# Optimization experiments

Hardware: AMD Instinct MI355X
Metric: run time of the kernel (lower is better)

Reference implementation:

```python
import jax, jax.numpy as jnp
import numpy as np

B, N, U = 16, 1024, 64  # batch, nodes, num_units
ALPHA = 0.2  # LeakyReLU negative slope
NEG = -9e15


def setup_inputs() -> dict:
    key = jax.random.key(0)
    ks = jax.random.split(key, 7)
    X = jax.random.normal(ks[0], (B, N, U), dtype=jnp.float32)
    state = jax.random.normal(ks[1], (B, N, U), dtype=jnp.float32)
    # random sparse adjacency (avg degree ~32) with self-loops
    adj = (jax.random.uniform(ks[2], (N, N)) < 32.0 / N).astype(jnp.float32)
    adj = jnp.maximum(adj, jnp.eye(N, dtype=jnp.float32))
    def xavier(k, shape):
        fan_in, fan_out = shape
        s = 1.414 * np.sqrt(6.0 / (fan_in + fan_out))
        return jax.random.uniform(k, shape, jnp.float32, -s, s)
    W1 = xavier(ks[3], (2 * U, 2 * U))   # gat_1: in 2U -> out 2U
    a1 = xavier(ks[4], (4 * U, 1))       # attention vector, 2*out
    W2 = xavier(ks[5], (2 * U, U))       # gat_2: in 2U -> out U
    a2 = xavier(ks[6], (2 * U, 1))
    return {"X": X, "state": state, "adj": adj, "W1": W1, "a1": a1, "W2": W2, "a2": a2}


def _gat_layer(x, adj, W, a):
    # x: [b,n,f_in], W: [f_in,F], a: [2F,1]
    h = jnp.einsum('bnf,fo->bno', x, W)              # [b,n,F]
    F_out = W.shape[1]
    s_src = h @ a[:F_out, 0]                         # [b,n] contribution of node i
    s_dst = h @ a[F_out:, 0]                         # [b,n] contribution of node j
    e = jax.nn.leaky_relu(s_src[:, :, None] + s_dst[:, None, :], ALPHA)  # [b,n,n]
    e = jnp.where(adj[None, :, :] > 0, e, NEG)
    att = jax.nn.softmax(e, axis=2)                  # masked softmax over neighbors j
    return jnp.einsum('bij,bjf->bif', att, h)        # [b,n,F]


def reference(X, state, adj, W1, a1, W2, a2):
    X1 = jnp.concatenate([X, state], axis=2)         # [b,n,2U]
    gv = jax.nn.sigmoid(_gat_layer(X1, adj, W1, a1)) # [b,n,2U]
    r, z = jnp.split(gv, 2, axis=2)                  # each [b,n,U]
    X2 = jnp.concatenate([X, r * state], axis=2)
    h_t1 = jnp.tanh(_gat_layer(X2, adj, W2, a2))     # [b,n,U]
    new_h = z * state + (1.0 - z) * h_t1
    return new_h
```

## Files before the change

kernel.cpp:

```cpp
#include <hip/hip_runtime.h>

#define BB 16
#define NN 1024
#define LALPHA 0.2f
#define MAXD 192

__global__ void build_csr(const float* __restrict__ adj, int* __restrict__ deg,
                          int* __restrict__ cols) {
    __shared__ int cnt;
    int i = blockIdx.x;
    if (threadIdx.x == 0) cnt = 0;
    __syncthreads();
    for (int j = threadIdx.x; j < NN; j += blockDim.x) {
        if (adj[(size_t)i * NN + j] > 0.0f) {
            int p = atomicAdd(&cnt, 1);
            if (p < MAXD) cols[(size_t)i * MAXD + p] = j;
        }
    }
    __syncthreads();
    if (threadIdx.x == 0) deg[i] = cnt < MAXD ? cnt : MAXD;
}

template <int FOUT, int RB>
__global__ void gemm_score(const float* __restrict__ A0, const float* __restrict__ A1,
                           const float* __restrict__ W, const float* __restrict__ avec,
                           float* __restrict__ h, float* __restrict__ s_src,
                           float* __restrict__ s_dst) {
    constexpr int TFN = FOUT / 4;
    constexpr int NT = (RB / 4) * TFN;
    __shared__ float xs[RB][132];
    int t = threadIdx.x;
    int tf = t % TFN, tr = t / TFN;
    int f0 = tf * 4, r0 = tr * 4;
    int base = blockIdx.x * RB;

    for (int idx = t; idx < RB * 32; idx += NT) {
        int r = idx >> 5, c = (idx & 31) * 4;
        float4 v = (c < 64) ? *(const float4*)(A0 + (size_t)(base + r) * 64 + c)
                            : *(const float4*)(A1 + (size_t)(base + r) * 64 + (c - 64));
        xs[r][c] = v.x; xs[r][c + 1] = v.y; xs[r][c + 2] = v.z; xs[r][c + 3] = v.w;
    }
    __syncthreads();

    float acc[4][4] = {};
    for (int k = 0; k < 128; k += 4) {
        float4 xv[4], wv[4];
#pragma unroll
        for (int i = 0; i < 4; i++) xv[i] = *(const float4*)&xs[r0 + i][k];
#pragma unroll
        for (int i = 0; i < 4; i++) wv[i] = *(const float4*)(W + (size_t)(k + i) * FOUT + f0);
#pragma unroll
        for (int i = 0; i < 4; i++) {
            float xr[4] = {xv[i].x, xv[i].y, xv[i].z, xv[i].w};
#pragma unroll
            for (int kk = 0; kk < 4; kk++) {
                acc[i][0] += xr[kk] * wv[kk].x;
                acc[i][1] += xr[kk] * wv[kk].y;
                acc[i][2] += xr[kk] * wv[kk].z;
                acc[i][3] += xr[kk] * wv[kk].w;
            }
        }
    }

    float a_s[4], a_d[4];
#pragma unroll
    for (int i = 0; i < 4; i++) {
        a_s[i] = avec[f0 + i];
        a_d[i] = avec[FOUT + f0 + i];
    }
#pragma unroll
    for (int i = 0; i < 4; i++) {
        int m = base + r0 + i;
        *(float4*)(h + (size_t)m * FOUT + f0) =
            make_float4(acc[i][0], acc[i][1], acc[i][2], acc[i][3]);
        float ps = acc[i][0] * a_s[0] + acc[i][1] * a_s[1] + acc[i][2] * a_s[2] + acc[i][3] * a_s[3];
        float pd = acc[i][0] * a_d[0] + acc[i][1] * a_d[1] + acc[i][2] * a_d[2] + acc[i][3] * a_d[3];
#pragma unroll
        for (int o = TFN / 2; o >= 1; o >>= 1) {
            ps += __shfl_xor(ps, o);
            pd += __shfl_xor(pd, o);
        }
        if (tf == 0) {
            s_src[m] = ps;
            s_dst[m] = pd;
        }
    }
}

__global__ __launch_bounds__(256) void attn1_kernel(
    const int* __restrict__ deg, const int* __restrict__ cols,
    const float* __restrict__ h1, const float* __restrict__ s_src,
    const float* __restrict__ s_dst, const float* __restrict__ state,
    float* __restrict__ rstate, float* __restrict__ zbuf) {
    int wv = threadIdx.x >> 6;
    int lane = threadIdx.x & 63;
    int node = wv >> 1;
    int half = wv & 1;
    int bi = blockIdx.x * 2 + node;
    int i = bi & (NN - 1);
    int b = bi >> 10;
    int d = deg[i];
    float ssrc = s_src[bi];
    __shared__ float w[2][MAXD];
    __shared__ int cl[2][MAXD];

    float ev[3];
    float mx = -1e30f;
    int nslot = 0;
    for (int j = lane; j < d; j += 64, nslot++) {
        int c = cols[(size_t)i * MAXD + j];
        cl[node][j] = c;
        float e = ssrc + s_dst[b * NN + c];
        e = e > 0.f ? e : LALPHA * e;
        ev[nslot] = e;
        mx = fmaxf(mx, e);
    }
#pragma unroll
    for (int o = 32; o >= 1; o >>= 1) mx = fmaxf(mx, __shfl_xor(mx, o));
    float sum = 0.f;
    {
        int s = 0;
        for (int j = lane; j < d; j += 64, s++) {
            float p = __expf(ev[s] - mx);
            sum += p;
            w[node][j] = p;
        }
    }
#pragma unroll
    for (int o = 32; o >= 1; o >>= 1) sum += __shfl_xor(sum, o);
    float inv = 1.f / sum;

    const float* hb = h1 + (size_t)b * NN * 128 + half * 64;
    float acc = 0.f;
    int j = 0;
    for (; j + 1 < d; j += 2) {
        float w0 = w[node][j], w1 = w[node][j + 1];
        const float* p0 = hb + (size_t)cl[node][j] * 128;
        const float* p1 = hb + (size_t)cl[node][j + 1] * 128;
        acc += w0 * p0[lane] + w1 * p1[lane];
    }
    if (j < d) acc += w[node][j] * (hb + (size_t)cl[node][j] * 128)[lane];

    float g = 1.f / (1.f + __expf(-acc * inv));
    float st = state[(size_t)bi * 64 + lane];
    if (half == 0)
        rstate[(size_t)bi * 64 + lane] = g * st;
    else
        zbuf[(size_t)bi * 64 + lane] = g;
}

__global__ __launch_bounds__(256) void attn2_kernel(
    const int* __restrict__ deg, const int* __restrict__ cols,
    const float* __restrict__ h2, const float* __restrict__ s_src,
    const float* __restrict__ s_dst, const float* __restrict__ state,
    const float* __restrict__ zbuf, float* __restrict__ out) {
    int wv = threadIdx.x >> 6;
    int lane = threadIdx.x & 63;
    int node = wv >> 1;
    int half = wv & 1;
    int bi = blockIdx.x * 2 + node;
    int i = bi & (NN - 1);
    int b = bi >> 10;
    int d = deg[i];
    float ssrc = s_src[bi];
    __shared__ float w[2][MAXD];
    __shared__ int cl[2][MAXD];
    __shared__ float part[2][64];

    float ev[3];
    float mx = -1e30f;
    int nslot = 0;
    for (int j = lane; j < d; j += 64, nslot++) {
        int c = cols[(size_t)i * MAXD + j];
        cl[node][j] = c;
        float e = ssrc + s_dst[b * NN + c];
        e = e > 0.f ? e : LALPHA * e;
        ev[nslot] = e;
        mx = fmaxf(mx, e);
    }
#pragma unroll
    for (int o = 32; o >= 1; o >>= 1) mx = fmaxf(mx, __shfl_xor(mx, o));
    float sum = 0.f;
    {
        int s = 0;
        for (int j = lane; j < d; j += 64, s++) {
            float p = __expf(ev[s] - mx);
            sum += p;
            w[node][j] = p;
        }
    }
#pragma unroll
    for (int o = 32; o >= 1; o >>= 1) sum += __shfl_xor(sum, o);
    float inv = 1.f / sum;

    const float* hb = h2 + (size_t)b * NN * 64;
    float acc = 0.f;
    int j = half;
    for (; j + 2 < d; j += 4) {
        float w0 = w[node][j], w1 = w[node][j + 2];
        const float* p0 = hb + (size_t)cl[node][j] * 64;
        const float* p1 = hb + (size_t)cl[node][j + 2] * 64;
        acc += w0 * p0[lane] + w1 * p1[lane];
    }
    for (; j < d; j += 2) acc += w[node][j] * (hb + (size_t)cl[node][j] * 64)[lane];

    if (half == 1) part[node][lane] = acc;
    __syncthreads();
    if (half == 0) {
        acc += part[node][lane];
        float ht = tanhf(acc * inv);
        float z = zbuf[(size_t)bi * 64 + lane];
        float st = state[(size_t)bi * 64 + lane];
        out[(size_t)bi * 64 + lane] = z * st + (1.f - z) * ht;
    }
}

extern "C" void kernel_launch(void* const* d_in, const int* in_sizes, int n_in,
                              void* d_out, int out_size, void* d_ws, size_t ws_size,
                              hipStream_t stream) {
    const float* X     = (const float*)d_in[0];
    const float* state = (const float*)d_in[1];
    const float* adj   = (const float*)d_in[2];
    const float* W1    = (const float*)d_in[3];
    const float* a1    = (const float*)d_in[4];
    const float* W2    = (const float*)d_in[5];
    const float* a2    = (const float*)d_in[6];
    float* out = (float*)d_out;

    char* ws = (char*)d_ws;
    size_t off = 0;
    auto alloc = [&](size_t bytes) -> void* {
        void* p = ws + off;
        off = (off + bytes + 255) & ~(size_t)255;
        return p;
    };
    int*   deg    = (int*)alloc(NN * sizeof(int));
    int*   cols   = (int*)alloc((size_t)NN * MAXD * sizeof(int));
    float* h1     = (float*)alloc((size_t)BB * NN * 128 * sizeof(float));
    float* ssrc1  = (float*)alloc((size_t)BB * NN * sizeof(float));
    float* sdst1  = (float*)alloc((size_t)BB * NN * sizeof(float));
    float* rstate = (float*)alloc((size_t)BB * NN * 64 * sizeof(float));
    float* zbuf   = (float*)alloc((size_t)BB * NN * 64 * sizeof(float));
    float* h2     = (float*)alloc((size_t)BB * NN * 64 * sizeof(float));
    float* ssrc2  = (float*)alloc((size_t)BB * NN * sizeof(float));
    float* sdst2  = (float*)alloc((size_t)BB * NN * sizeof(float));

    const int M = BB * NN;

    build_csr<<<NN, 256, 0, stream>>>(adj, deg, cols);
    gemm_score<128, 32><<<M / 32, 256, 0, stream>>>(X, state, W1, a1, h1, ssrc1, sdst1);
    attn1_kernel<<<M / 2, 256, 0, stream>>>(deg, cols, h1, ssrc1, sdst1, state, rstate, zbuf);
    gemm_score<64, 64><<<M / 64, 256, 0, stream>>>(X, rstate, W2, a2, h2, ssrc2, sdst2);
    attn2_kernel<<<M / 2, 256, 0, stream>>>(deg, cols, h2, ssrc2, sdst2, state, zbuf, out);
}
```

Measured before the change: 160.2 us.

## Use one wave per node with float2 feature loads in attention kernels

Reassigns each node to a single 64-lane wave instead of two waves, with each lane accumulating two features via float2 loads. Pads neighbor lists to a multiple of four with zero weights to unroll the gather loop by four. This removes duplicated softmax computation across waves and widens memory accesses, at the cost of fewer concurrent waves per node and a block-level sync.

```diff
diff --git a/kernel.cpp b/kernel.cpp
--- a/kernel.cpp
+++ b/kernel.cpp
@@ -87,131 +87,138 @@
     }
 }
 
-__global__ __launch_bounds__(256) void attn1_kernel(
+__global__ __launch_bounds__(64) void attn1_kernel(
     const int* __restrict__ deg, const int* __restrict__ cols,
     const float* __restrict__ h1, const float* __restrict__ s_src,
     const float* __restrict__ s_dst, const float* __restrict__ state,
     float* __restrict__ rstate, float* __restrict__ zbuf) {
-    int wv = threadIdx.x >> 6;
-    int lane = threadIdx.x & 63;
-    int node = wv >> 1;
-    int half = wv & 1;
-    int bi = blockIdx.x * 2 + node;
+    int bi = blockIdx.x;
     int i = bi & (NN - 1);
     int b = bi >> 10;
+    int lane = threadIdx.x;
     int d = deg[i];
     float ssrc = s_src[bi];
-    __shared__ float w[2][MAXD];
-    __shared__ int cl[2][MAXD];
+    __shared__ float w[MAXD + 4];
+    __shared__ int cl[MAXD + 4];
 
     float ev[3];
     float mx = -1e30f;
-    int nslot = 0;
-    for (int j = lane; j < d; j += 64, nslot++) {
+    int s = 0;
+    for (int j = lane; j < d; j += 64, s++) {
         int c = cols[(size_t)i * MAXD + j];
-        cl[node][j] = c;
+        cl[j] = c;
         float e = ssrc + s_dst[b * NN + c];
         e = e > 0.f ? e : LALPHA * e;
-        ev[nslot] = e;
+        ev[s] = e;
         mx = fmaxf(mx, e);
     }
 #pragma unroll
     for (int o = 32; o >= 1; o >>= 1) mx = fmaxf(mx, __shfl_xor(mx, o));
     float sum = 0.f;
-    {
-        int s = 0;
-        for (int j = lane; j < d; j += 64, s++) {
-            float p = __expf(ev[s] - mx);
-            sum += p;
-            w[node][j] = p;
-        }
+    s = 0;
+    for (int j = lane; j < d; j += 64, s++) {
+        float p = __expf(ev[s] - mx);
+        w[j] = p;
+        sum += p;
     }
 #pragma unroll
     for (int o = 32; o >= 1; o >>= 1) sum += __shfl_xor(sum, o);
+    if (lane < 4) {
+        w[d + lane] = 0.f;
+        cl[d + lane] = 0;
+    }
+    __syncthreads();
     float inv = 1.f / sum;
 
-    const float* hb = h1 + (size_t)b * NN * 128 + half * 64;
-    float acc = 0.f;
-    int j = 0;
-    for (; j + 1 < d; j += 2) {
-        float w0 = w[node][j], w1 = w[node][j + 1];
-        const float* p0 = hb + (size_t)cl[node][j] * 128;
-        const float* p1 = hb + (size_t)cl[node][j + 1] * 128;
-        acc += w0 * p0[lane] + w1 * p1[lane];
-    }
-    if (j < d) acc += w[node][j] * (hb + (size_t)cl[node][j] * 128)[lane];
-
-    float g = 1.f / (1.f + __expf(-acc * inv));
-    float st = state[(size_t)bi * 64 + lane];
-    if (half == 0)
-        rstate[(size_t)bi * 64 + lane] = g * st;
-    else
-        zbuf[(size_t)bi * 64 + lane] = g;
-}
-
-__global__ __launch_bounds__(256) void attn2_kernel(
+    const float* hb = h1 + (size_t)b * NN * 128 + lane * 2;
+    int de4 = (d + 3) & ~3;
+    float ax = 0.f, ay = 0.f;
+    for (int j = 0; j < de4; j += 4) {
+        float2 r0 = *(const float2*)(hb + (size_t)cl[j] * 128);
+        float2 r1 = *(const float2*)(hb + (size_t)cl[j + 1] * 128);
+        float2 r2 = *(const float2*)(hb + (size_t)cl[j + 2] * 128);
+        float2 r3 = *(const float2*)(hb + (size_t)cl[j + 3] * 128);
+        float w0 = w[j], w1 = w[j + 1], w2 = w[j + 2], w3 = w[j + 3];
+        ax += w0 * r0.x + w1 * r1.x + w2 * r2.x + w3 * r3.x;
+        ay += w0 * r0.y + w1 * r1.y + w2 * r2.y + w3 * r3.y;
+    }
+    float gx = 1.f / (1.f + __expf(-ax * inv));
+    float gy = 1.f / (1.f + __expf(-ay * inv));
+    if (lane < 32) {
+        float2 st = *(const float2*)(state + (size_t)bi * 64 + lane * 2);
+        *(float2*)(rstate + (size_t)bi * 64 + lane * 2) = make_float2(gx * st.x, gy * st.y);
+    } else {
+        int l2 = lane - 32;
+        *(float2*)(zbuf + (size_t)bi * 64 + l2 * 2) = make_float2(gx, gy);
+    }
+}
+
+__global__ __launch_bounds__(64) void attn2_kernel(
     const int* __restrict__ deg, const int* __restrict__ cols,
     const float* __restrict__ h2, const float* __restrict__ s_src,
     const float* __restrict__ s_dst, const float* __restrict__ state,
     const float* __restrict__ zbuf, float* __restrict__ out) {
-    int wv = threadIdx.x >> 6;
-    int lane = threadIdx.x & 63;
-    int node = wv >> 1;
-    int half = wv & 1;
-    int bi = blockIdx.x * 2 + node;
+    int bi = blockIdx.x;
     int i = bi & (NN - 1);
     int b = bi >> 10;
+    int lane = threadIdx.x;
+    int half = lane >> 5;
+    int fl = lane & 31;
     int d = deg[i];
     float ssrc = s_src[bi];
-    __shared__ float w[2][MAXD];
-    __shared__ int cl[2][MAXD];
-    __shared__ float part[2][64];
+    __shared__ float w[MAXD + 4];
+    __shared__ int cl[MAXD + 4];
 
     float ev[3];
     float mx = -1e30f;
-    int nslot = 0;
-    for (int j = lane; j < d; j += 64, nslot++) {
+    int s = 0;
+    for (int j = lane; j < d; j += 64, s++) {
         int c = cols[(size_t)i * MAXD + j];
-        cl[node][j] = c;
+        cl[j] = c;
         float e = ssrc + s_dst[b * NN + c];
         e = e > 0.f ? e : LALPHA * e;
-        ev[nslot] = e;
+        ev[s] = e;
         mx = fmaxf(mx, e);
     }
 #pragma unroll
     for (int o = 32; o >= 1; o >>= 1) mx = fmaxf(mx, __shfl_xor(mx, o));
     float sum = 0.f;
-    {
-        int s = 0;
-        for (int j = lane; j < d; j += 64, s++) {
-            float p = __expf(ev[s] - mx);
-            sum += p;
-            w[node][j] = p;
-        }
+    s = 0;
+    for (int j = lane; j < d; j += 64, s++) {
+        float p = __expf(ev[s] - mx);
+        w[j] = p;
+        sum += p;
     }
 #pragma unroll
     for (int o = 32; o >= 1; o >>= 1) sum += __shfl_xor(sum, o);
+    if (lane < 4) {
+        w[d + lane] = 0.f;
+        cl[d + lane] = 0;
+    }
+    __syncthreads();
     float inv = 1.f / sum;
 
-    const float* hb = h2 + (size_t)b * NN * 64;
-    float acc = 0.f;
-    int j = half;
-    for (; j + 2 < d; j += 4) {
-        float w0 = w[node][j], w1 = w[node][j + 2];
-        const float* p0 = hb + (size_t)cl[node][j] * 64;
-        const float* p1 = hb + (size_t)cl[node][j + 2] * 64;
-        acc += w0 * p0[lane] + w1 * p1[lane];
-    }
-    for (; j < d; j += 2) acc += w[node][j] * (hb + (size_t)cl[node][j] * 64)[lane];
-
-    if (half == 1) part[node][lane] = acc;
-    __syncthreads();
-    if (half == 0) {
-        acc += part[node][lane];
-        float ht = tanhf(acc * inv);
-        float z = zbuf[(size_t)bi * 64 + lane];
-        float st = state[(size_t)bi * 64 + lane];
-        out[(size_t)bi * 64 + lane] = z * st + (1.f - z) * ht;
+    const float* hb = h2 + (size_t)b * NN * 64 + fl * 2;
+    int de4 = (d + 3) & ~3;
+    float ax = 0.f, ay = 0.f;
+    for (int j = 0; j < de4; j += 4) {
+        int i0 = j + half, i1 = j + 2 + half;
+        float2 r0 = *(const float2*)(hb + (size_t)cl[i0] * 64);
+        float2 r1 = *(const float2*)(hb + (size_t)cl[i1] * 64);
+        float w0 = w[i0], w1 = w[i1];
+        ax += w0 * r0.x + w1 * r1.x;
+        ay += w0 * r0.y + w1 * r1.y;
+    }
+    ax += __shfl_xor(ax, 32);
+    ay += __shfl_xor(ay, 32);
+    if (lane < 32) {
+        float hx = tanhf(ax * inv);
+        float hy = tanhf(ay * inv);
+        float2 z2 = *(const float2*)(zbuf + (size_t)bi * 64 + lane * 2);
+        float2 st = *(const float2*)(state + (size_t)bi * 64 + lane * 2);
+        *(float2*)(out + (size_t)bi * 64 + lane * 2) =
+            make_float2(z2.x * st.x + (1.f - z2.x) * hx,
+                        z2.y * st.y + (1.f - z2.y) * hy);
     }
 }
 
@@ -249,7 +256,7 @@
 
     build_csr<<<NN, 256, 0, stream>>>(adj, deg, cols);
     gemm_score<128, 32><<<M / 32, 256, 0, stream>>>(X, state, W1, a1, h1, ssrc1, sdst1);
-    attn1_kernel<<<M / 2, 256, 0, stream>>>(deg, cols, h1, ssrc1, sdst1, state, rstate, zbuf);
+    attn1_kernel<<<M, 64, 0, stream>>>(deg, cols, h1, ssrc1, sdst1, state, rstate, zbuf);
     gemm_score<64, 64><<<M / 64, 256, 0, stream>>>(X, rstate, W2, a2, h2, ssrc2, sdst2);
-    attn2_kernel<<<M / 2, 256, 0, stream>>>(deg, cols, h2, ssrc2, sdst2, state, zbuf, out);
-}
+    attn2_kernel<<<M, 64, 0, stream>>>(deg, cols, h2, ssrc2, sdst2, state, zbuf, out);
+}
```

Result: faster. 146.9 us (-8.3%).
